# Optimization experiments

Measured on AMD Instinct MI355X. Metric: run time of the kernel, lower is better.

The kernel has to match this reference:

```python
import jax, jax.numpy as jnp
import numpy as np

INPUT_SIZE = 16
K = 50
HIDDEN_COUNT = 25
FINAL_WIDTH = INPUT_SIZE + HIDDEN_COUNT * K  # 1266


def setup_inputs() -> dict:
    key = jax.random.key(0)
    k1, k2, k3, k4, k5 = jax.random.split(key, 5)
    B = 32768
    state = jax.random.normal(k1, (B, INPUT_SIZE), dtype=jnp.float32)
    # Zero-padded weight stack: layer i uses Ws[i, :, : INPUT_SIZE + i*K]
    Ws = jax.random.normal(k2, (HIDDEN_COUNT, K, FINAL_WIDTH), dtype=jnp.float32) * 0.05
    bs = jax.random.normal(k3, (HIDDEN_COUNT, K), dtype=jnp.float32) * 0.05
    Wout = jax.random.normal(k4, (FINAL_WIDTH, 1), dtype=jnp.float32) * 0.05
    bout = jax.random.normal(k5, (1,), dtype=jnp.float32) * 0.05
    return {"state": state, "Ws": Ws, "bs": bs, "Wout": Wout, "bout": bout}


def reference(state, Ws, bs, Wout, bout):
    x = state  # [B, 16], grows by 50 per layer
    for i in range(HIDDEN_COUNT):  # fixed-size structural loop over layers
        width = INPUT_SIZE + i * K
        w = Ws[i, :, :width]                       # [50, width] (static slice)
        y = jax.nn.leaky_relu(x @ w.T + bs[i], negative_slope=0.01)  # [B, 50]
        x = jnp.concatenate([x, y], axis=1)        # [B, width+50]
    return x @ Wout + bout  # [B, 1]
```

## Files before the change

kernel.cpp:

```cpp
#include <hip/hip_runtime.h>


#define IN 16
#define KJ 50
#define NL 25
#define FW 1266
#define TR 24
#define NB 1366
#define BTOT 32768
#define XSTR 1288
#define NTHREADS 512
#define XLO_OFF 61824
#define SLAB_OFF 123648
#define LDS_BYTES 148224
#define CHUNK_STRIDE 3200
#define TOTAL_CHUNKS 973

typedef __attribute__((ext_vector_type(8))) short bf16x8;
typedef __attribute__((ext_vector_type(16))) float f32x16;

__device__ __forceinline__ unsigned short bf16_hi(float x, float* hif) {
    unsigned u = __float_as_uint(x);
    unsigned h = (u + 0x8000u) >> 16;
    *hif = __uint_as_float(h << 16);
    return (unsigned short)h;
}
__device__ __forceinline__ unsigned short bf16_rnd(float x) {
    return (unsigned short)((__float_as_uint(x) + 0x8000u) >> 16);
}

__device__ __forceinline__ void split8(const float* __restrict__ rowp, int kb, int width,
                                       unsigned hi[4], unsigned lo[4]) {
#pragma unroll
    for (int p = 0; p < 4; ++p) {
        unsigned h2[2], l2[2];
#pragma unroll
        for (int q = 0; q < 2; ++q) {
            int k = kb + p * 2 + q;
            float v = (k < width) ? rowp[k] : 0.f;
            float hif;
            unsigned short h = bf16_hi(v, &hif);
            h2[q] = h;
            l2[q] = bf16_rnd(v - hif);
        }
        hi[p] = h2[0] | (h2[1] << 16);
        lo[p] = l2[0] | (l2[1] << 16);
    }
}

__global__ __launch_bounds__(64, 1) void split_w(const float* __restrict__ Ws,
                                                 char* __restrict__ wsbuf) {
    int rem = blockIdx.x, layer = 0;
    size_t off = 0;
    for (;;) {
        int c = (IN + KJ * layer + 15) >> 4;
        if (rem < c) break;
        rem -= c; off += (size_t)c * CHUNK_STRIDE; ++layer;
    }
    const int ci = rem, k0 = ci << 4, width = IN + KJ * layer;
    const float* Wl = Ws + (size_t)layer * KJ * FW;
    char* base = wsbuf + off + (size_t)ci * CHUNK_STRIDE;
    const int l = threadIdx.x, ll = l & 31, kh = l >> 5;
    const int kb = k0 + kh * 8;

    unsigned hi[4], lo[4];
    split8(Wl + (size_t)ll * FW, kb, width, hi, lo);
    *reinterpret_cast<uint4*>(base + l * 16)        = make_uint4(hi[0], hi[1], hi[2], hi[3]);
    *reinterpret_cast<uint4*>(base + 1024 + l * 16) = make_uint4(lo[0], lo[1], lo[2], lo[3]);
    if (ll < 18) {
        split8(Wl + (size_t)(32 + ll) * FW, kb, width, hi, lo);
        *reinterpret_cast<uint4*>(base + 2048 + (kh * 18 + ll) * 16) = make_uint4(hi[0], hi[1], hi[2], hi[3]);
        *reinterpret_cast<uint4*>(base + 2624 + (kh * 18 + ll) * 16) = make_uint4(lo[0], lo[1], lo[2], lo[3]);
    }
}

__device__ __forceinline__ void loadB(const char* __restrict__ wb, int ci, int n,
                                      int l, int ll, int kh, bf16x8& bh, bf16x8& bl) {
    const char* cb = wb + (size_t)ci * CHUNK_STRIDE;
    if (n == 0) {
        bh = *(const bf16x8*)(cb + l * 16);
        bl = *(const bf16x8*)(cb + 1024 + l * 16);
    } else {
        bf16x8 z = {0, 0, 0, 0, 0, 0, 0, 0};
        bh = z; bl = z;
        if (ll < 18) {
            bh = *(const bf16x8*)(cb + 2048 + (kh * 18 + ll) * 16);
            bl = *(const bf16x8*)(cb + 2624 + (kh * 18 + ll) * 16);
        }
    }
}

__global__ __launch_bounds__(NTHREADS, 1) void densenet_mfma(
    const float* __restrict__ state, const char* __restrict__ wsbuf,
    const float* __restrict__ bs,    const float* __restrict__ Wout,
    const float* __restrict__ bout,  float* __restrict__ out)
{
    __shared__ __align__(16) char lds[LDS_BYTES];
    unsigned short* xhi = (unsigned short*)lds;
    unsigned short* xlo = (unsigned short*)(lds + XLO_OFF);
    float* slab = (float*)(lds + SLAB_OFF);

    const int tid = threadIdx.x;
    const int w   = tid >> 6;
    const int l   = tid & 63;
    const int ll  = l & 31, kh = l >> 5;
    const int kq  = w & 3;
    const int n   = w >> 2;
    const long row0 = (long)blockIdx.x * TR;

    {
        unsigned* p = (unsigned*)lds;
        for (int i = tid; i < (XLO_OFF * 2) / 4; i += NTHREADS) p[i] = 0u;
    }
    __syncthreads();
    if (tid < TR * IN) {
        int r = tid >> 4, c = tid & 15;
        if (row0 + r < BTOT) {
            float v = state[(row0 + r) * IN + c];
            float hif;
            xhi[r * XSTR + c] = bf16_hi(v, &hif);
            xlo[r * XSTR + c] = bf16_rnd(v - hif);
        }
    }
    __syncthreads();

    int width = IN;
    size_t wofs = 0;
    for (int layer = 0; layer < NL; ++layer) {
        const int chunks = (width + 15) >> 4;
        const char* wb = wsbuf + wofs;

        f32x16 acc;
#pragma unroll
        for (int i = 0; i < 16; ++i) acc[i] = 0.f;

        bf16x8 h0 = {0,0,0,0,0,0,0,0}, l0v = h0, h1 = h0, l1v = h0;
        if (kq < chunks)     loadB(wb, kq,     n, l, ll, kh, h0, l0v);
        if (kq + 4 < chunks) loadB(wb, kq + 4, n, l, ll, kh, h1, l1v);
        for (int ci = kq; ci < chunks; ci += 8) {
            {
                const int kof = (ci << 4) + (kh << 3);
                bf16x8 ah = *(const bf16x8*)&xhi[ll * XSTR + kof];
                bf16x8 al = *(const bf16x8*)&xlo[ll * XSTR + kof];
                acc = __builtin_amdgcn_mfma_f32_32x32x16_bf16(al, h0, acc, 0, 0, 0);
                acc = __builtin_amdgcn_mfma_f32_32x32x16_bf16(ah, l0v, acc, 0, 0, 0);
                acc = __builtin_amdgcn_mfma_f32_32x32x16_bf16(ah, h0, acc, 0, 0, 0);
            }
            if (ci + 8 < chunks) loadB(wb, ci + 8, n, l, ll, kh, h0, l0v);
            if (ci + 4 < chunks) {
                const int kof = ((ci + 4) << 4) + (kh << 3);
                bf16x8 ah = *(const bf16x8*)&xhi[ll * XSTR + kof];
                bf16x8 al = *(const bf16x8*)&xlo[ll * XSTR + kof];
                acc = __builtin_amdgcn_mfma_f32_32x32x16_bf16(al, h1, acc, 0, 0, 0);
                acc = __builtin_amdgcn_mfma_f32_32x32x16_bf16(ah, l1v, acc, 0, 0, 0);
                acc = __builtin_amdgcn_mfma_f32_32x32x16_bf16(ah, h1, acc, 0, 0, 0);
                if (ci + 12 < chunks) loadB(wb, ci + 12, n, l, ll, kh, h1, l1v);
            }
        }

        {
            float* sl = slab + kq * 1536;
#pragma unroll
            for (int r = 0; r < 12; ++r) {
                int crow = (r & 3) + 8 * (r >> 2) + 4 * kh;
                sl[crow * 64 + n * 32 + ll] = acc[r];
            }
        }
        __syncthreads();

#pragma unroll
        for (int it = 0; it < 3; ++it) {
            int idx = it * NTHREADS + tid;
            int row = idx >> 6, j = idx & 63;
            float s = slab[row * 64 + j] + slab[1536 + row * 64 + j]
                    + slab[3072 + row * 64 + j] + slab[4608 + row * 64 + j];
            if (j < KJ) {
                s += bs[layer * KJ + j];
                s = (s > 0.f) ? s : 0.01f * s;
                float hif;
                xhi[row * XSTR + width + j] = bf16_hi(s, &hif);
                xlo[row * XSTR + width + j] = bf16_rnd(s - hif);
            }
        }
        __syncthreads();

        width += KJ;
        wofs += (size_t)chunks * CHUNK_STRIDE;
    }

#pragma unroll
    for (int rr = 0; rr < 3; ++rr) {
        const int row = w * 3 + rr;
        const long grow = row0 + row;
        float s = 0.f;
        for (int k = l; k < FW; k += 64) {
            float xv = __uint_as_float((unsigned)xhi[row * XSTR + k] << 16)
                     + __uint_as_float((unsigned)xlo[row * XSTR + k] << 16);
            s += xv * Wout[k];
        }
#pragma unroll
        for (int m = 32; m >= 1; m >>= 1) s += __shfl_xor(s, m, 64);
        if (l == 0 && grow < BTOT) out[grow] = s + bout[0];
    }
}

extern "C" void kernel_launch(void* const* d_in, const int* in_sizes, int n_in,
                              void* d_out, int out_size, void* d_ws, size_t ws_size,
                              hipStream_t stream) {
    const float* state = (const float*)d_in[0];
    const float* Ws    = (const float*)d_in[1];
    const float* bs    = (const float*)d_in[2];
    const float* Wout  = (const float*)d_in[3];
    const float* bout  = (const float*)d_in[4];
    float* out = (float*)d_out;
    char* wsbuf = (char*)d_ws;

    split_w<<<dim3(TOTAL_CHUNKS), dim3(64), 0, stream>>>(Ws, wsbuf);
    densenet_mfma<<<dim3(NB), dim3(NTHREADS), 0, stream>>>(state, wsbuf, bs, Wout, bout, out);
}
```

Baseline: 550.5 us.

## Split MFMA accumulation into four chains with grouped weight prefetch and LDS-staged Wout/bias

The inner K loop now keeps four independent accumulators and prefetches weight fragments two chunk-pairs ahead. This breaks the single serial MFMA dependency chain and hides global load latency. Wout and the biases are copied into LDS once per block, and the output dot product is fully unrolled. The loop rounds up to whole groups, so it issues some MFMAs on zero-filled fragments. The launch bound now asks for two blocks per CU, which can limit registers and cause spills while the LDS footprint still allows only one block.

```diff
diff --git a/kernel.cpp b/kernel.cpp
--- a/kernel.cpp
+++ b/kernel.cpp
@@ -12,7 +12,9 @@
 #define NTHREADS 512
 #define XLO_OFF 61824
 #define SLAB_OFF 123648
-#define LDS_BYTES 148224
+#define WOUT_OFF 148224
+#define BIAS_OFF 153344
+#define LDS_BYTES 158464
 #define CHUNK_STRIDE 3200
 #define TOTAL_CHUNKS 973
 
@@ -74,23 +76,39 @@
     }
 }
 
-__device__ __forceinline__ void loadB(const char* __restrict__ wb, int ci, int n,
-                                      int l, int ll, int kh, bf16x8& bh, bf16x8& bl) {
-    const char* cb = wb + (size_t)ci * CHUNK_STRIDE;
-    if (n == 0) {
-        bh = *(const bf16x8*)(cb + l * 16);
-        bl = *(const bf16x8*)(cb + 1024 + l * 16);
-    } else {
-        bf16x8 z = {0, 0, 0, 0, 0, 0, 0, 0};
-        bh = z; bl = z;
-        if (ll < 18) {
-            bh = *(const bf16x8*)(cb + 2048 + (kh * 18 + ll) * 16);
-            bl = *(const bf16x8*)(cb + 2624 + (kh * 18 + ll) * 16);
-        }
-    }
-}
-
-__global__ __launch_bounds__(NTHREADS, 1) void densenet_mfma(
+__device__ __forceinline__ void loadB2(const char* __restrict__ wb, int ci, int chunks,
+                                       int n, int l, int ll, int kh,
+                                       bf16x8& bh, bf16x8& bl) {
+    bf16x8 z = {0, 0, 0, 0, 0, 0, 0, 0};
+    bh = z; bl = z;
+    if (ci < chunks) {
+        const char* cb = wb + (size_t)ci * CHUNK_STRIDE;
+        if (n == 0) {
+            bh = *(const bf16x8*)(cb + l * 16);
+            bl = *(const bf16x8*)(cb + 1024 + l * 16);
+        } else if (ll < 18) {
+            bh = *(const bf16x8*)(cb + (kh * 18 + ll) * 16);
+            bl = *(const bf16x8*)(cb + 576 + (kh * 18 + ll) * 16);
+        }
+    }
+}
+__device__ __forceinline__ void loadG2(const char* __restrict__ wb, int c0, int chunks,
+                                       int n, int l, int ll, int kh,
+                                       bf16x8& b0h, bf16x8& b0l, bf16x8& b1h, bf16x8& b1l) {
+    loadB2(wb, c0,     chunks, n, l, ll, kh, b0h, b0l);
+    loadB2(wb, c0 + 4, chunks, n, l, ll, kh, b1h, b1l);
+}
+
+__device__ __forceinline__ void mfma3(const unsigned short* xrh, const unsigned short* xrl,
+                                      int kof, const bf16x8 bh, const bf16x8 bl, f32x16& acc) {
+    bf16x8 ah = *(const bf16x8*)(xrh + kof);
+    bf16x8 al = *(const bf16x8*)(xrl + kof);
+    acc = __builtin_amdgcn_mfma_f32_32x32x16_bf16(al, bh, acc, 0, 0, 0);
+    acc = __builtin_amdgcn_mfma_f32_32x32x16_bf16(ah, bl, acc, 0, 0, 0);
+    acc = __builtin_amdgcn_mfma_f32_32x32x16_bf16(ah, bh, acc, 0, 0, 0);
+}
+
+__global__ __launch_bounds__(NTHREADS, 2) void densenet_mfma(
     const float* __restrict__ state, const char* __restrict__ wsbuf,
     const float* __restrict__ bs,    const float* __restrict__ Wout,
     const float* __restrict__ bout,  float* __restrict__ out)
@@ -98,7 +116,9 @@
     __shared__ __align__(16) char lds[LDS_BYTES];
     unsigned short* xhi = (unsigned short*)lds;
     unsigned short* xlo = (unsigned short*)(lds + XLO_OFF);
-    float* slab = (float*)(lds + SLAB_OFF);
+    float* slab  = (float*)(lds + SLAB_OFF);
+    float* woutl = (float*)(lds + WOUT_OFF);
+    float* biasl = (float*)(lds + BIAS_OFF);
 
     const int tid = threadIdx.x;
     const int w   = tid >> 6;
@@ -112,6 +132,8 @@
         unsigned* p = (unsigned*)lds;
         for (int i = tid; i < (XLO_OFF * 2) / 4; i += NTHREADS) p[i] = 0u;
     }
+    for (int i = tid; i < FW; i += NTHREADS)      woutl[i] = Wout[i];
+    for (int i = tid; i < NL * KJ; i += NTHREADS) biasl[i] = bs[i];
     __syncthreads();
     if (tid < TR * IN) {
         int r = tid >> 4, c = tid & 15;
@@ -124,37 +146,35 @@
     }
     __syncthreads();
 
+    const unsigned short* xrh = xhi + ll * XSTR + (kh << 3);
+    const unsigned short* xrl = xlo + ll * XSTR + (kh << 3);
+
     int width = IN;
     size_t wofs = 0;
     for (int layer = 0; layer < NL; ++layer) {
         const int chunks = (width + 15) >> 4;
-        const char* wb = wsbuf + wofs;
-
-        f32x16 acc;
-#pragma unroll
-        for (int i = 0; i < 16; ++i) acc[i] = 0.f;
-
-        bf16x8 h0 = {0,0,0,0,0,0,0,0}, l0v = h0, h1 = h0, l1v = h0;
-        if (kq < chunks)     loadB(wb, kq,     n, l, ll, kh, h0, l0v);
-        if (kq + 4 < chunks) loadB(wb, kq + 4, n, l, ll, kh, h1, l1v);
-        for (int ci = kq; ci < chunks; ci += 8) {
-            {
-                const int kof = (ci << 4) + (kh << 3);
-                bf16x8 ah = *(const bf16x8*)&xhi[ll * XSTR + kof];
-                bf16x8 al = *(const bf16x8*)&xlo[ll * XSTR + kof];
-                acc = __builtin_amdgcn_mfma_f32_32x32x16_bf16(al, h0, acc, 0, 0, 0);
-                acc = __builtin_amdgcn_mfma_f32_32x32x16_bf16(ah, l0v, acc, 0, 0, 0);
-                acc = __builtin_amdgcn_mfma_f32_32x32x16_bf16(ah, h0, acc, 0, 0, 0);
-            }
-            if (ci + 8 < chunks) loadB(wb, ci + 8, n, l, ll, kh, h0, l0v);
-            if (ci + 4 < chunks) {
-                const int kof = ((ci + 4) << 4) + (kh << 3);
-                bf16x8 ah = *(const bf16x8*)&xhi[ll * XSTR + kof];
-                bf16x8 al = *(const bf16x8*)&xlo[ll * XSTR + kof];
-                acc = __builtin_amdgcn_mfma_f32_32x32x16_bf16(al, h1, acc, 0, 0, 0);
-                acc = __builtin_amdgcn_mfma_f32_32x32x16_bf16(ah, l1v, acc, 0, 0, 0);
-                acc = __builtin_amdgcn_mfma_f32_32x32x16_bf16(ah, h1, acc, 0, 0, 0);
-                if (ci + 12 < chunks) loadB(wb, ci + 12, n, l, ll, kh, h1, l1v);
+        const char* wb = wsbuf + wofs + (n ? 2048 : 0);
+
+        f32x16 a0, a1, a2, a3;
+#pragma unroll
+        for (int i = 0; i < 16; ++i) { a0[i] = 0.f; a1[i] = 0.f; a2[i] = 0.f; a3[i] = 0.f; }
+
+        const int T  = (chunks > kq) ? ((chunks - kq + 3) >> 2) : 0;
+        int NG = (T + 1) >> 1;
+        NG += (NG & 1);
+
+        if (NG > 0) {
+            bf16x8 A0h, A0l, A1h, A1l, B0h, B0l, B1h, B1l;
+            loadG2(wb, kq, chunks, n, l, ll, kh, A0h, A0l, A1h, A1l);
+            for (int G = 0; G < NG; G += 2) {
+                const int c0 = kq + (G << 3);
+                loadG2(wb, c0 + 8, chunks, n, l, ll, kh, B0h, B0l, B1h, B1l);
+                mfma3(xrh, xrl, (c0)     << 4, A0h, A0l, a0);
+                mfma3(xrh, xrl, (c0 + 4) << 4, A1h, A1l, a1);
+                if (G + 2 < NG)
+                    loadG2(wb, c0 + 16, chunks, n, l, ll, kh, A0h, A0l, A1h, A1l);
+                mfma3(xrh, xrl, (c0 + 8)  << 4, B0h, B0l, a2);
+                mfma3(xrh, xrl, (c0 + 12) << 4, B1h, B1l, a3);
             }
         }
 
@@ -162,8 +182,9 @@
             float* sl = slab + kq * 1536;
 #pragma unroll
             for (int r = 0; r < 12; ++r) {
+                float v = (a0[r] + a1[r]) + (a2[r] + a3[r]);
                 int crow = (r & 3) + 8 * (r >> 2) + 4 * kh;
-                sl[crow * 64 + n * 32 + ll] = acc[r];
+                sl[crow * 64 + n * 32 + ll] = v;
             }
         }
         __syncthreads();
@@ -172,10 +193,10 @@
         for (int it = 0; it < 3; ++it) {
             int idx = it * NTHREADS + tid;
             int row = idx >> 6, j = idx & 63;
-            float s = slab[row * 64 + j] + slab[1536 + row * 64 + j]
-                    + slab[3072 + row * 64 + j] + slab[4608 + row * 64 + j];
+            float s = (slab[row * 64 + j] + slab[1536 + row * 64 + j])
+                    + (slab[3072 + row * 64 + j] + slab[4608 + row * 64 + j]);
             if (j < KJ) {
-                s += bs[layer * KJ + j];
+                s += biasl[layer * KJ + j];
                 s = (s > 0.f) ? s : 0.01f * s;
                 float hif;
                 xhi[row * XSTR + width + j] = bf16_hi(s, &hif);
@@ -188,19 +209,32 @@
         wofs += (size_t)chunks * CHUNK_STRIDE;
     }
 
+    const float b0 = bout[0];
 #pragma unroll
     for (int rr = 0; rr < 3; ++rr) {
         const int row = w * 3 + rr;
         const long grow = row0 + row;
+        const unsigned short* xh = xhi + row * XSTR;
+        const unsigned short* xl = xlo + row * XSTR;
         float s = 0.f;
-        for (int k = l; k < FW; k += 64) {
-            float xv = __uint_as_float((unsigned)xhi[row * XSTR + k] << 16)
-                     + __uint_as_float((unsigned)xlo[row * XSTR + k] << 16);
-            s += xv * Wout[k];
+#pragma unroll
+        for (int it = 0; it < 19; ++it) {
+            int k = l + (it << 6);
+            float xv = __uint_as_float((unsigned)xh[k] << 16)
+                     + __uint_as_float((unsigned)xl[k] << 16);
+            s += xv * woutl[k];
+        }
+        {
+            int k = 1216 + l;
+            if (k < FW) {
+                float xv = __uint_as_float((unsigned)xh[k] << 16)
+                         + __uint_as_float((unsigned)xl[k] << 16);
+                s += xv * woutl[k];
+            }
         }
 #pragma unroll
         for (int m = 32; m >= 1; m >>= 1) s += __shfl_xor(s, m, 64);
-        if (l == 0 && grow < BTOT) out[grow] = s + bout[0];
+        if (l == 0 && grow < BTOT) out[grow] = s + b0;
     }
 }
 
```

Result: faster. 512.3 us (-6.9%).
